# Kernel tuning notes

Measured on AMD Instinct MI355X. Metric: run time of the kernel, lower is better.

Reference implementation:

```python
import jax, jax.numpy as jnp
import numpy as np

EPS = 1e-5  # torch BatchNorm1d default eps


def _bn_train(h, gamma, beta):
    # BatchNorm1d in training mode over the edge (batch) axes: biased variance.
    m = jnp.mean(h, axis=(0, 1), keepdims=True)
    v = jnp.mean(jnp.square(h - m), axis=(0, 1), keepdims=True)
    return (h - m) * jax.lax.rsqrt(v + EPS) * gamma + beta


def setup_inputs() -> dict:
    key = jax.random.key(0)
    ks = jax.random.split(key, 12)
    N, F, H = 1024, 128, 128
    s1 = 1.0 / np.sqrt(2 * F)
    s2 = 1.0 / np.sqrt(H)
    return {
        "x": jax.random.normal(ks[0], (N, F), dtype=jnp.float32),
        "W1": jax.random.uniform(ks[1], (H, 2 * F), jnp.float32, -s1, s1),
        "b1": jax.random.uniform(ks[2], (H,), jnp.float32, -s1, s1),
        "W2": jax.random.uniform(ks[3], (H, H), jnp.float32, -s2, s2),
        "b2": jax.random.uniform(ks[4], (H,), jnp.float32, -s2, s2),
        "W3": jax.random.uniform(ks[5], (1, H), jnp.float32, -s2, s2),
        "b3": jax.random.uniform(ks[6], (1,), jnp.float32, -s2, s2),
        "g1": jnp.ones((H,), jnp.float32),
        "be1": jnp.zeros((H,), jnp.float32),
        "g2": jnp.ones((H,), jnp.float32),
        "be2": jnp.zeros((H,), jnp.float32),
    }


def reference(x, W1, b1, W2, b2, W3, b3, g1, be1, g2, be2):
    N, F = x.shape
    # Edge e = i*N + j pairs [x[j], x[i]] (row=j varies fast, col=i slow).
    # First Linear on the concat splits into two low-rank GEMMs + broadcast add,
    # avoiding the [N^2, 2F] materialization (same math as Linear(concat)).
    Wa, Wb = W1[:, :F], W1[:, F:]
    A = x @ Wa.T            # contribution of x[row] = x[j] -> varies over axis 1
    B = x @ Wb.T            # contribution of x[col] = x[i] -> varies over axis 0
    h = A[None, :, :] + B[:, None, :] + b1      # [N, N, H], h[i, j]
    h = jax.nn.relu(_bn_train(h, g1, be1))
    h = jnp.einsum('ijh,kh->ijk', h, W2) + b2   # [N, N, H]
    h = jax.nn.relu(_bn_train(h, g2, be2))
    logits = jnp.einsum('ijh,kh->ijk', h, W3)[..., 0] + b3[0]  # [N, N]
    adj = jax.nn.sigmoid((logits + logits.T) * 0.5)
    adj = adj - jnp.diag(jnp.diag(adj))
    return adj
```

## Files before the change

### kernel.cpp

```cpp
#include <hip/hip_runtime.h>
#include <hip/hip_bf16.h>

typedef __bf16 bf16x8 __attribute__((ext_vector_type(8)));
typedef float  f32x4  __attribute__((ext_vector_type(4)));
typedef float  f32x8  __attribute__((ext_vector_type(8)));

#define EPSV 1e-5f

__global__ __launch_bounds__(256) void k_ab(const float* __restrict__ x,
                                            const float* __restrict__ W1,
                                            const float* __restrict__ W2,
                                            float* __restrict__ A,
                                            float* __restrict__ Bm,
                                            float* __restrict__ gs,
                                            unsigned int* __restrict__ w2p) {
  __shared__ float xs[4 * 128];
  int t = threadIdx.x;
  if (blockIdx.x >= 256) {
    int c = (blockIdx.x - 256) * 256 + t;
    int pair = c & 3;
    int col  = (c >> 2) & 15;
    int quad = (c >> 6) & 3;
    int nt   = (c >> 8) & 7;
    int ks   = (c >> 11) & 3;
    int k = nt * 16 + col;
    int hch = ks * 32 + quad * 8 + pair * 2;
    __bf16 b0 = (__bf16)W2[k * 128 + hch];
    __bf16 b1 = (__bf16)W2[k * 128 + hch + 1];
    unsigned int u0 = *(unsigned short*)&b0, u1 = *(unsigned short*)&b1;
    w2p[c] = u0 | (u1 << 16);
    return;
  }
  int j0 = blockIdx.x * 4;
  for (int idx = t; idx < 512; idx += 256) xs[idx] = x[j0 * 128 + idx];
  __syncthreads();
  int h = t & 127, half = t >> 7;
  const float4* wrow = (const float4*)(W1 + h * 256 + half * 128);
  const float4* xs4 = (const float4*)xs;
  float a0 = 0.f, a1 = 0.f, a2 = 0.f, a3 = 0.f;
#pragma unroll 8
  for (int ch = 0; ch < 32; ++ch) {
    float4 wv = wrow[ch];
    float4 x0 = xs4[ch], x1 = xs4[32 + ch], x2 = xs4[64 + ch], x3 = xs4[96 + ch];
    a0 += wv.x * x0.x + wv.y * x0.y + wv.z * x0.z + wv.w * x0.w;
    a1 += wv.x * x1.x + wv.y * x1.y + wv.z * x1.z + wv.w * x1.w;
    a2 += wv.x * x2.x + wv.y * x2.y + wv.z * x2.z + wv.w * x2.w;
    a3 += wv.x * x3.x + wv.y * x3.y + wv.z * x3.z + wv.w * x3.w;
  }
  float* dst = half ? Bm : A;
  dst[(j0 + 0) * 128 + h] = a0;
  dst[(j0 + 1) * 128 + h] = a1;
  dst[(j0 + 2) * 128 + h] = a2;
  dst[(j0 + 3) * 128 + h] = a3;
  float s = a0 + a1 + a2 + a3;
  float q = a0 * a0 + a1 * a1 + a2 * a2 + a3 * a3;
  atomicAdd(&gs[half * 256 + h], s);
  atomicAdd(&gs[half * 256 + 128 + h], q);
}

__global__ __launch_bounds__(256) void k_fold_apply(const float* __restrict__ gs,
                                                    const float* __restrict__ g1,
                                                    const float* __restrict__ be1,
                                                    const float* __restrict__ A,
                                                    const float* __restrict__ Bm,
                                                    float* __restrict__ Ap,
                                                    float* __restrict__ Bt) {
  __shared__ float sc_s[128], ta_s[128], tb_s[128];
  int t = threadIdx.x;
  if (t < 128) {
    const float inv = 1.f / 1024.f;
    float mA = gs[t] * inv;
    float vA = gs[128 + t] * inv - mA * mA;
    float mB = gs[256 + t] * inv;
    float vB = gs[384 + t] * inv - mB * mB;
    float sc = g1[t] * rsqrtf(vA + vB + EPSV);
    sc_s[t] = sc;
    ta_s[t] = be1[t] - mA * sc;
    tb_s[t] = -mB * sc;
  }
  __syncthreads();
  int idx4 = blockIdx.x * 256 + t;
  int c4 = idx4 & 31;
  float4 sc = ((const float4*)sc_s)[c4];
  float4 ta = ((const float4*)ta_s)[c4];
  float4 tb = ((const float4*)tb_s)[c4];
  float4 a = ((const float4*)A)[idx4];
  float4 b = ((const float4*)Bm)[idx4];
  float4 oa, ob;
  oa.x = fmaf(a.x, sc.x, ta.x); oa.y = fmaf(a.y, sc.y, ta.y);
  oa.z = fmaf(a.z, sc.z, ta.z); oa.w = fmaf(a.w, sc.w, ta.w);
  ob.x = fmaf(b.x, sc.x, tb.x); ob.y = fmaf(b.y, sc.y, tb.y);
  ob.z = fmaf(b.z, sc.z, tb.z); ob.w = fmaf(b.w, sc.w, tb.w);
  int j = idx4 >> 5;
  int h4 = c4 << 2;
  int S = j >> 6, r = (j >> 4) & 3, col = j & 15;
  int ks = h4 >> 5, q = (h4 >> 3) & 3, eh = (h4 >> 2) & 1;
  int dst4 = S * 2048 + eh * 1024 + (r * 4 + ks) * 64 + q * 16 + col;
  ((float4*)Ap)[dst4] = oa;
  ((float4*)Bt)[idx4] = ob;
}

__device__ __forceinline__ bf16x8 build2(f32x4 alo, f32x4 ahi,
                                         const float* __restrict__ bp) {
  f32x4 b0 = *(const f32x4*)bp;
  f32x4 b1 = *(const f32x4*)(bp + 4);
  f32x4 z = {0.f, 0.f, 0.f, 0.f};
  f32x4 h0 = __builtin_elementwise_max(alo + b0, z);
  f32x4 h1 = __builtin_elementwise_max(ahi + b1, z);
  f32x8 h = __builtin_shufflevector(h0, h1, 0, 1, 2, 3, 4, 5, 6, 7);
  return __builtin_convertvector(h, bf16x8);
}

template <int PASS>
__global__ __launch_bounds__(256) void k_pass(
    const float* __restrict__ Ap, const float* __restrict__ Bt,
    const unsigned int* __restrict__ w2p, float* __restrict__ partials,
    const float* __restrict__ sum2, const float* __restrict__ g2,
    const float* __restrict__ be2, const float* __restrict__ W3v,
    const float* __restrict__ b3p, float* __restrict__ L) {
  __shared__ float lds[8192 + 1024];
  float* btl = lds + 8192;
  int t = threadIdx.x;
  int bid = blockIdx.x;
  int bj = bid & 15, bi = bid >> 4;
  int lane = t & 63, w = t >> 6;
  int col = lane & 15, quad = lane >> 4;

  const float* atsrc = Ap + bj * 8192;
#pragma unroll
  for (int it = 0; it < 8; ++it) {
    int g = w * 8 + it;
    __builtin_amdgcn_global_load_lds(
        (const __attribute__((address_space(1))) unsigned int*)(atsrc + g * 256 + lane * 4),
        (__attribute__((address_space(3))) unsigned int*)(lds + g * 256),
        16, 0, 0);
  }
  __builtin_amdgcn_global_load_lds(
      (const __attribute__((address_space(1))) unsigned int*)(Bt + (bi * 8 + w * 2) * 128 + lane * 4),
      (__attribute__((address_space(3))) unsigned int*)(btl + w * 256),
      16, 0, 0);

  bf16x8 bw[4][8];
#pragma unroll
  for (int ks = 0; ks < 4; ++ks)
#pragma unroll
    for (int nt = 0; nt < 8; ++nt)
      bw[ks][nt] = *(const bf16x8*)((const __bf16*)w2p + (((ks * 8 + nt) * 64) + lane) * 8);

  float s1[8], s2[8];
  float al[8], uu[8], w3l[8];
  float b3v = 0.f;
  if (PASS == 1) {
#pragma unroll
    for (int nt = 0; nt < 8; ++nt) { s1[nt] = 0.f; s2[nt] = 0.f; }
  } else {
    b3v = b3p[0];
    const float invM = 1.f / (1024.f * 1024.f);
#pragma unroll
    for (int nt = 0; nt < 8; ++nt) {
      int k = nt * 16 + col;
      float mdot = sum2[k] * invM;
      float var = sum2[128 + k] * invM - mdot * mdot;
      float alv = g2[k] * rsqrtf(var + EPSV);
      al[nt] = alv;
      uu[nt] = be2[k] - mdot * alv;
      w3l[nt] = W3v[k];
    }
  }
  __syncthreads();

  const float* bp0 = btl + w * 256;
  const float* bp1 = bp0 + 128;

  for (int s = 0; s < 4; ++s) {
    f32x4 acc[2][8];
#pragma unroll
    for (int mt = 0; mt < 2; ++mt)
#pragma unroll
      for (int nt = 0; nt < 8; ++nt) acc[mt][nt] = (f32x4){0.f, 0.f, 0.f, 0.f};

#pragma unroll
    for (int ks = 0; ks < 4; ++ks) {
      const float* ap = lds + ((s * 4 + ks) * 64 + lane) * 4;
      f32x4 alo = *(const f32x4*)ap;
      f32x4 ahi = *(const f32x4*)(ap + 4096);
      bf16x8 a0 = build2(alo, ahi, bp0 + ks * 32 + quad * 8);
      bf16x8 a1 = build2(alo, ahi, bp1 + ks * 32 + quad * 8);
#pragma unroll
      for (int nt = 0; nt < 8; ++nt) {
        acc[0][nt] = __builtin_amdgcn_mfma_f32_16x16x32_bf16(a0, bw[ks][nt], acc[0][nt], 0, 0, 0);
        acc[1][nt] = __builtin_amdgcn_mfma_f32_16x16x32_bf16(a1, bw[ks][nt], acc[1][nt], 0, 0, 0);
      }
    }

    if (PASS == 1) {
#pragma unroll
      for (int nt = 0; nt < 8; ++nt)
#pragma unroll
        for (int mt = 0; mt < 2; ++mt)
#pragma unroll
          for (int r = 0; r < 4; ++r) {
            float d = acc[mt][nt][r];
            s1[nt] += d;
            s2[nt] = fmaf(d, d, s2[nt]);
          }
    } else {
#pragma unroll
      for (int mt = 0; mt < 2; ++mt) {
        float rsum[4] = {0.f, 0.f, 0.f, 0.f};
#pragma unroll
        for (int nt = 0; nt < 8; ++nt)
#pragma unroll
          for (int r = 0; r < 4; ++r) {
            float h = fmaxf(fmaf(acc[mt][nt][r], al[nt], uu[nt]), 0.f);
            rsum[r] = fmaf(h, w3l[nt], rsum[r]);
          }
#pragma unroll
        for (int r = 0; r < 4; ++r) {
          rsum[r] += __shfl_xor(rsum[r], 1);
          rsum[r] += __shfl_xor(rsum[r], 2);
          rsum[r] += __shfl_xor(rsum[r], 4);
          rsum[r] += __shfl_xor(rsum[r], 8);
        }
        if (col == 0) {
          int i = bi * 8 + w * 2 + mt;
#pragma unroll
          for (int r = 0; r < 4; ++r)
            L[i * 1024 + bj * 64 + s * 16 + quad * 4 + r] = rsum[r] + b3v;
        }
      }
    }
  }

  if (PASS == 1) {
#pragma unroll
    for (int nt = 0; nt < 8; ++nt) {
      s1[nt] += __shfl_xor(s1[nt], 16);
      s1[nt] += __shfl_xor(s1[nt], 32);
      s2[nt] += __shfl_xor(s2[nt], 16);
      s2[nt] += __shfl_xor(s2[nt], 32);
    }
    __syncthreads();
    if (lane < 16) {
#pragma unroll
      for (int nt = 0; nt < 8; ++nt) {
        lds[w * 256 + nt * 16 + lane] = s1[nt];
        lds[w * 256 + 128 + nt * 16 + lane] = s2[nt];
      }
    }
    __syncthreads();
    float tot = lds[t] + lds[256 + t] + lds[512 + t] + lds[768 + t];
    partials[bid * 256 + t] = tot;
  }
}

__global__ __launch_bounds__(256) void k_red_partials(const float* __restrict__ partials,
                                                      float* __restrict__ sum2) {
  int t = threadIdx.x;
  float s = 0.f;
  int r0 = blockIdx.x * 16;
#pragma unroll
  for (int r = 0; r < 16; ++r) s += partials[(r0 + r) * 256 + t];
  atomicAdd(&sum2[t], s);
}

__global__ __launch_bounds__(256) void k_adj(const float* __restrict__ L,
                                             float* __restrict__ out) {
  int idx = blockIdx.x * 256 + threadIdx.x;
  int i = idx >> 10, j = idx & 1023;
  float a = L[i * 1024 + j];
  float b = L[j * 1024 + i];
  float s = 1.f / (1.f + __expf(-0.5f * (a + b)));
  out[idx] = (i == j) ? 0.f : s;
}

extern "C" void kernel_launch(void* const* d_in, const int* in_sizes, int n_in,
                              void* d_out, int out_size, void* d_ws, size_t ws_size,
                              hipStream_t stream) {
  const float* x   = (const float*)d_in[0];
  const float* W1  = (const float*)d_in[1];
  const float* W2  = (const float*)d_in[3];
  const float* W3  = (const float*)d_in[5];
  const float* b3  = (const float*)d_in[6];
  const float* g1  = (const float*)d_in[7];
  const float* be1 = (const float*)d_in[8];
  const float* g2  = (const float*)d_in[9];
  const float* be2 = (const float*)d_in[10];

  float* ws = (float*)d_ws;
  float* A        = ws;
  float* Bm       = ws + 131072;
  float* Ap       = ws + 262144;
  float* Bt       = ws + 393216;
  unsigned int* w2p = (unsigned int*)(ws + 524288);
  float* gs       = ws + 532480;
  float* sum2     = ws + 532992;
  float* partials = ws + 533248;
  float* L        = ws + 1057536;
  float* out      = (float*)d_out;

  hipMemsetAsync(gs, 0, 768 * sizeof(float), stream);

  k_ab<<<288, 256, 0, stream>>>(x, W1, W2, A, Bm, gs, w2p);
  k_fold_apply<<<128, 256, 0, stream>>>(gs, g1, be1, A, Bm, Ap, Bt);
  k_pass<1><<<2048, 256, 0, stream>>>(Ap, Bt, w2p, partials, nullptr, nullptr, nullptr, nullptr, nullptr, nullptr);
  k_red_partials<<<128, 256, 0, stream>>>(partials, sum2);
  k_pass<2><<<2048, 256, 0, stream>>>(Ap, Bt, w2p, nullptr, sum2, g2, be2, W3, b3, L);
  k_adj<<<4096, 256, 0, stream>>>(L, out);
}
```

Measured before the change: 225.3 us.

## Keep Bt rows in registers as packed bf16 and prefetch A fragments

Measured after the change: 229.8 us. No clear change (+2.0%).

```diff
diff --git a/kernel.cpp b/kernel.cpp
--- a/kernel.cpp
+++ b/kernel.cpp
@@ -100,13 +100,19 @@
   ((float4*)Bt)[idx4] = ob;
 }
 
-__device__ __forceinline__ bf16x8 build2(f32x4 alo, f32x4 ahi,
-                                         const float* __restrict__ bp) {
-  f32x4 b0 = *(const f32x4*)bp;
-  f32x4 b1 = *(const f32x4*)(bp + 4);
+__device__ __forceinline__ bf16x8 build_bt(f32x4 alo, f32x4 ahi, uint4 bt) {
+  f32x4 blo, bhi;
+  blo[0] = __uint_as_float(bt.x << 16);
+  blo[1] = __uint_as_float(bt.x & 0xffff0000u);
+  blo[2] = __uint_as_float(bt.y << 16);
+  blo[3] = __uint_as_float(bt.y & 0xffff0000u);
+  bhi[0] = __uint_as_float(bt.z << 16);
+  bhi[1] = __uint_as_float(bt.z & 0xffff0000u);
+  bhi[2] = __uint_as_float(bt.w << 16);
+  bhi[3] = __uint_as_float(bt.w & 0xffff0000u);
   f32x4 z = {0.f, 0.f, 0.f, 0.f};
-  f32x4 h0 = __builtin_elementwise_max(alo + b0, z);
-  f32x4 h1 = __builtin_elementwise_max(ahi + b1, z);
+  f32x4 h0 = __builtin_elementwise_max(alo + blo, z);
+  f32x4 h1 = __builtin_elementwise_max(ahi + bhi, z);
   f32x8 h = __builtin_shufflevector(h0, h1, 0, 1, 2, 3, 4, 5, 6, 7);
   return __builtin_convertvector(h, bf16x8);
 }
@@ -118,8 +124,7 @@
     const float* __restrict__ sum2, const float* __restrict__ g2,
     const float* __restrict__ be2, const float* __restrict__ W3v,
     const float* __restrict__ b3p, float* __restrict__ L) {
-  __shared__ float lds[8192 + 1024];
-  float* btl = lds + 8192;
+  __shared__ float lds[8192];
   int t = threadIdx.x;
   int bid = blockIdx.x;
   int bj = bid & 15, bi = bid >> 4;
@@ -135,10 +140,21 @@
         (__attribute__((address_space(3))) unsigned int*)(lds + g * 256),
         16, 0, 0);
   }
-  __builtin_amdgcn_global_load_lds(
-      (const __attribute__((address_space(1))) unsigned int*)(Bt + (bi * 8 + w * 2) * 128 + lane * 4),
-      (__attribute__((address_space(3))) unsigned int*)(btl + w * 256),
-      16, 0, 0);
+
+  uint4 btu[2][4];
+  {
+    const float* br = Bt + (bi * 8 + w * 2) * 128;
+#pragma unroll
+    for (int r = 0; r < 2; ++r)
+#pragma unroll
+      for (int ks = 0; ks < 4; ++ks) {
+        f32x4 lo = *(const f32x4*)(br + r * 128 + ks * 32 + quad * 8);
+        f32x4 hi = *(const f32x4*)(br + r * 128 + ks * 32 + quad * 8 + 4);
+        f32x8 v = __builtin_shufflevector(lo, hi, 0, 1, 2, 3, 4, 5, 6, 7);
+        bf16x8 b = __builtin_convertvector(v, bf16x8);
+        btu[r][ks] = *(uint4*)&b;
+      }
+  }
 
   bf16x8 bw[4][8];
 #pragma unroll
@@ -169,9 +185,6 @@
   }
   __syncthreads();
 
-  const float* bp0 = btl + w * 256;
-  const float* bp1 = bp0 + 128;
-
   for (int s = 0; s < 4; ++s) {
     f32x4 acc[2][8];
 #pragma unroll
@@ -179,18 +192,26 @@
 #pragma unroll
       for (int nt = 0; nt < 8; ++nt) acc[mt][nt] = (f32x4){0.f, 0.f, 0.f, 0.f};
 
+    const float* ap0 = lds + (s * 4 * 64 + lane) * 4;
+    f32x4 alo = *(const f32x4*)ap0;
+    f32x4 ahi = *(const f32x4*)(ap0 + 4096);
 #pragma unroll
     for (int ks = 0; ks < 4; ++ks) {
-      const float* ap = lds + ((s * 4 + ks) * 64 + lane) * 4;
-      f32x4 alo = *(const f32x4*)ap;
-      f32x4 ahi = *(const f32x4*)(ap + 4096);
-      bf16x8 a0 = build2(alo, ahi, bp0 + ks * 32 + quad * 8);
-      bf16x8 a1 = build2(alo, ahi, bp1 + ks * 32 + quad * 8);
+      f32x4 nlo, nhi;
+      if (ks < 3) {
+        const float* apn = lds + (((s * 4 + ks + 1) * 64) + lane) * 4;
+        nlo = *(const f32x4*)apn;
+        nhi = *(const f32x4*)(apn + 4096);
+      }
+      bf16x8 a0 = build_bt(alo, ahi, btu[0][ks]);
+      bf16x8 a1 = build_bt(alo, ahi, btu[1][ks]);
 #pragma unroll
       for (int nt = 0; nt < 8; ++nt) {
         acc[0][nt] = __builtin_amdgcn_mfma_f32_16x16x32_bf16(a0, bw[ks][nt], acc[0][nt], 0, 0, 0);
         acc[1][nt] = __builtin_amdgcn_mfma_f32_16x16x32_bf16(a1, bw[ks][nt], acc[1][nt], 0, 0, 0);
       }
+      alo = nlo;
+      ahi = nhi;
     }
 
     if (PASS == 1) {
```

## Fuse BN1 fold into pass kernels and replace partials reduction with atomics

Applied to the files above, without the earlier changes.

Result: slower. 246.4 us (+9.4%).

```diff
diff --git a/kernel.cpp b/kernel.cpp
--- a/kernel.cpp
+++ b/kernel.cpp
@@ -10,7 +10,7 @@
 __global__ __launch_bounds__(256) void k_ab(const float* __restrict__ x,
                                             const float* __restrict__ W1,
                                             const float* __restrict__ W2,
-                                            float* __restrict__ A,
+                                            float* __restrict__ Ap,
                                             float* __restrict__ Bm,
                                             float* __restrict__ gs,
                                             unsigned int* __restrict__ w2p) {
@@ -47,26 +47,71 @@
     a2 += wv.x * x2.x + wv.y * x2.y + wv.z * x2.z + wv.w * x2.w;
     a3 += wv.x * x3.x + wv.y * x3.y + wv.z * x3.z + wv.w * x3.w;
   }
-  float* dst = half ? Bm : A;
-  dst[(j0 + 0) * 128 + h] = a0;
-  dst[(j0 + 1) * 128 + h] = a1;
-  dst[(j0 + 2) * 128 + h] = a2;
-  dst[(j0 + 3) * 128 + h] = a3;
+  if (half == 0) {
+    int S = j0 >> 6, r16 = (j0 >> 4) & 3, colj = j0 & 15;
+    int ks = h >> 5, q = (h >> 3) & 3, eh = (h >> 2) & 1, pos = h & 3;
+    int base = S * 8192 + eh * 4096 + (r16 * 4 + ks) * 256 + q * 64 + colj * 4 + pos;
+    Ap[base] = a0;
+    Ap[base + 4] = a1;
+    Ap[base + 8] = a2;
+    Ap[base + 12] = a3;
+  } else {
+    Bm[(j0 + 0) * 128 + h] = a0;
+    Bm[(j0 + 1) * 128 + h] = a1;
+    Bm[(j0 + 2) * 128 + h] = a2;
+    Bm[(j0 + 3) * 128 + h] = a3;
+  }
   float s = a0 + a1 + a2 + a3;
-  float q = a0 * a0 + a1 * a1 + a2 * a2 + a3 * a3;
+  float q2 = a0 * a0 + a1 * a1 + a2 * a2 + a3 * a3;
   atomicAdd(&gs[half * 256 + h], s);
-  atomicAdd(&gs[half * 256 + 128 + h], q);
-}
-
-__global__ __launch_bounds__(256) void k_fold_apply(const float* __restrict__ gs,
-                                                    const float* __restrict__ g1,
-                                                    const float* __restrict__ be1,
-                                                    const float* __restrict__ A,
-                                                    const float* __restrict__ Bm,
-                                                    float* __restrict__ Ap,
-                                                    float* __restrict__ Bt) {
-  __shared__ float sc_s[128], ta_s[128], tb_s[128];
+  atomicAdd(&gs[half * 256 + 128 + h], q2);
+}
+
+__device__ __forceinline__ bf16x8 build_fold(f32x4 alo, f32x4 ahi,
+                                             const float* __restrict__ bp,
+                                             f32x4 sl, f32x4 sh,
+                                             f32x4 tl, f32x4 th) {
+  f32x4 b0 = *(const f32x4*)bp;
+  f32x4 b1 = *(const f32x4*)(bp + 4);
+  f32x4 z = {0.f, 0.f, 0.f, 0.f};
+  f32x4 h0 = __builtin_elementwise_max((alo + b0) * sl + tl, z);
+  f32x4 h1 = __builtin_elementwise_max((ahi + b1) * sh + th, z);
+  f32x8 h = __builtin_shufflevector(h0, h1, 0, 1, 2, 3, 4, 5, 6, 7);
+  return __builtin_convertvector(h, bf16x8);
+}
+
+template <int PASS>
+__global__ __launch_bounds__(256) void k_pass(
+    const float* __restrict__ Ap, const float* __restrict__ Bm,
+    const unsigned int* __restrict__ w2p,
+    const float* __restrict__ gs, const float* __restrict__ g1,
+    const float* __restrict__ be1,
+    float* __restrict__ sum2, const float* __restrict__ g2,
+    const float* __restrict__ be2, const float* __restrict__ W3v,
+    const float* __restrict__ b3p, float* __restrict__ L) {
+  __shared__ float lds[8192 + 1024 + 256];
+  float* btl = lds + 8192;
+  float* prm = lds + 9216;
   int t = threadIdx.x;
+  int bid = blockIdx.x;
+  int bj = bid & 15, bi = bid >> 4;
+  int lane = t & 63, w = t >> 6;
+  int col = lane & 15, quad = lane >> 4;
+
+  const float* atsrc = Ap + bj * 8192;
+#pragma unroll
+  for (int it = 0; it < 8; ++it) {
+    int g = w * 8 + it;
+    __builtin_amdgcn_global_load_lds(
+        (const __attribute__((address_space(1))) unsigned int*)(atsrc + g * 256 + lane * 4),
+        (__attribute__((address_space(3))) unsigned int*)(lds + g * 256),
+        16, 0, 0);
+  }
+  __builtin_amdgcn_global_load_lds(
+      (const __attribute__((address_space(1))) unsigned int*)(Bm + (bi * 8 + w * 2) * 128 + lane * 4),
+      (__attribute__((address_space(3))) unsigned int*)(btl + w * 256),
+      16, 0, 0);
+
   if (t < 128) {
     const float inv = 1.f / 1024.f;
     float mA = gs[t] * inv;
@@ -74,71 +119,9 @@
     float mB = gs[256 + t] * inv;
     float vB = gs[384 + t] * inv - mB * mB;
     float sc = g1[t] * rsqrtf(vA + vB + EPSV);
-    sc_s[t] = sc;
-    ta_s[t] = be1[t] - mA * sc;
-    tb_s[t] = -mB * sc;
-  }
-  __syncthreads();
-  int idx4 = blockIdx.x * 256 + t;
-  int c4 = idx4 & 31;
-  float4 sc = ((const float4*)sc_s)[c4];
-  float4 ta = ((const float4*)ta_s)[c4];
-  float4 tb = ((const float4*)tb_s)[c4];
-  float4 a = ((const float4*)A)[idx4];
-  float4 b = ((const float4*)Bm)[idx4];
-  float4 oa, ob;
-  oa.x = fmaf(a.x, sc.x, ta.x); oa.y = fmaf(a.y, sc.y, ta.y);
-  oa.z = fmaf(a.z, sc.z, ta.z); oa.w = fmaf(a.w, sc.w, ta.w);
-  ob.x = fmaf(b.x, sc.x, tb.x); ob.y = fmaf(b.y, sc.y, tb.y);
-  ob.z = fmaf(b.z, sc.z, tb.z); ob.w = fmaf(b.w, sc.w, tb.w);
-  int j = idx4 >> 5;
-  int h4 = c4 << 2;
-  int S = j >> 6, r = (j >> 4) & 3, col = j & 15;
-  int ks = h4 >> 5, q = (h4 >> 3) & 3, eh = (h4 >> 2) & 1;
-  int dst4 = S * 2048 + eh * 1024 + (r * 4 + ks) * 64 + q * 16 + col;
-  ((float4*)Ap)[dst4] = oa;
-  ((float4*)Bt)[idx4] = ob;
-}
-
-__device__ __forceinline__ bf16x8 build2(f32x4 alo, f32x4 ahi,
-                                         const float* __restrict__ bp) {
-  f32x4 b0 = *(const f32x4*)bp;
-  f32x4 b1 = *(const f32x4*)(bp + 4);
-  f32x4 z = {0.f, 0.f, 0.f, 0.f};
-  f32x4 h0 = __builtin_elementwise_max(alo + b0, z);
-  f32x4 h1 = __builtin_elementwise_max(ahi + b1, z);
-  f32x8 h = __builtin_shufflevector(h0, h1, 0, 1, 2, 3, 4, 5, 6, 7);
-  return __builtin_convertvector(h, bf16x8);
-}
-
-template <int PASS>
-__global__ __launch_bounds__(256) void k_pass(
-    const float* __restrict__ Ap, const float* __restrict__ Bt,
-    const unsigned int* __restrict__ w2p, float* __restrict__ partials,
-    const float* __restrict__ sum2, const float* __restrict__ g2,
-    const float* __restrict__ be2, const float* __restrict__ W3v,
-    const float* __restrict__ b3p, float* __restrict__ L) {
-  __shared__ float lds[8192 + 1024];
-  float* btl = lds + 8192;
-  int t = threadIdx.x;
-  int bid = blockIdx.x;
-  int bj = bid & 15, bi = bid >> 4;
-  int lane = t & 63, w = t >> 6;
-  int col = lane & 15, quad = lane >> 4;
-
-  const float* atsrc = Ap + bj * 8192;
-#pragma unroll
-  for (int it = 0; it < 8; ++it) {
-    int g = w * 8 + it;
-    __builtin_amdgcn_global_load_lds(
-        (const __attribute__((address_space(1))) unsigned int*)(atsrc + g * 256 + lane * 4),
-        (__attribute__((address_space(3))) unsigned int*)(lds + g * 256),
-        16, 0, 0);
-  }
-  __builtin_amdgcn_global_load_lds(
-      (const __attribute__((address_space(1))) unsigned int*)(Bt + (bi * 8 + w * 2) * 128 + lane * 4),
-      (__attribute__((address_space(3))) unsigned int*)(btl + w * 256),
-      16, 0, 0);
+    prm[t] = sc;
+    prm[128 + t] = be1[t] - (mA + mB) * sc;
+  }
 
   bf16x8 bw[4][8];
 #pragma unroll
@@ -184,8 +167,13 @@
       const float* ap = lds + ((s * 4 + ks) * 64 + lane) * 4;
       f32x4 alo = *(const f32x4*)ap;
       f32x4 ahi = *(const f32x4*)(ap + 4096);
-      bf16x8 a0 = build2(alo, ahi, bp0 + ks * 32 + quad * 8);
-      bf16x8 a1 = build2(alo, ahi, bp1 + ks * 32 + quad * 8);
+      int po = ks * 32 + quad * 8;
+      f32x4 sl = *(const f32x4*)(prm + po);
+      f32x4 sh = *(const f32x4*)(prm + po + 4);
+      f32x4 tl = *(const f32x4*)(prm + 128 + po);
+      f32x4 th = *(const f32x4*)(prm + 128 + po + 4);
+      bf16x8 a0 = build_fold(alo, ahi, bp0 + po, sl, sh, tl, th);
+      bf16x8 a1 = build_fold(alo, ahi, bp1 + po, sl, sh, tl, th);
 #pragma unroll
       for (int nt = 0; nt < 8; ++nt) {
         acc[0][nt] = __builtin_amdgcn_mfma_f32_16x16x32_bf16(a0, bw[ks][nt], acc[0][nt], 0, 0, 0);
@@ -224,9 +212,9 @@
         }
         if (col == 0) {
           int i = bi * 8 + w * 2 + mt;
-#pragma unroll
-          for (int r = 0; r < 4; ++r)
-            L[i * 1024 + bj * 64 + s * 16 + quad * 4 + r] = rsum[r] + b3v;
+          float4 v = make_float4(rsum[0] + b3v, rsum[1] + b3v,
+                                 rsum[2] + b3v, rsum[3] + b3v);
+          *(float4*)(&L[i * 1024 + bj * 64 + s * 16 + quad * 4]) = v;
         }
       }
     }
@@ -250,18 +238,8 @@
     }
     __syncthreads();
     float tot = lds[t] + lds[256 + t] + lds[512 + t] + lds[768 + t];
-    partials[bid * 256 + t] = tot;
-  }
-}
-
-__global__ __launch_bounds__(256) void k_red_partials(const float* __restrict__ partials,
-                                                      float* __restrict__ sum2) {
-  int t = threadIdx.x;
-  float s = 0.f;
-  int r0 = blockIdx.x * 16;
-#pragma unroll
-  for (int r = 0; r < 16; ++r) s += partials[(r0 + r) * 256 + t];
-  atomicAdd(&sum2[t], s);
+    atomicAdd(&sum2[t], tot);
+  }
 }
 
 __global__ __launch_bounds__(256) void k_adj(const float* __restrict__ L,
@@ -288,23 +266,20 @@
   const float* be2 = (const float*)d_in[10];
 
   float* ws = (float*)d_ws;
-  float* A        = ws;
+  float* Ap       = ws;
   float* Bm       = ws + 131072;
-  float* Ap       = ws + 262144;
-  float* Bt       = ws + 393216;
-  unsigned int* w2p = (unsigned int*)(ws + 524288);
-  float* gs       = ws + 532480;
-  float* sum2     = ws + 532992;
-  float* partials = ws + 533248;
-  float* L        = ws + 1057536;
+  unsigned int* w2p = (unsigned int*)(ws + 262144);
+  float* gs       = ws + 270336;
+  float* sum2     = ws + 270848;
+  float* L        = ws + 271104;
   float* out      = (float*)d_out;
 
   hipMemsetAsync(gs, 0, 768 * sizeof(float), stream);
 
-  k_ab<<<288, 256, 0, stream>>>(x, W1, W2, A, Bm, gs, w2p);
-  k_fold_apply<<<128, 256, 0, stream>>>(gs, g1, be1, A, Bm, Ap, Bt);
-  k_pass<1><<<2048, 256, 0, stream>>>(Ap, Bt, w2p, partials, nullptr, nullptr, nullptr, nullptr, nullptr, nullptr);
-  k_red_partials<<<128, 256, 0, stream>>>(partials, sum2);
-  k_pass<2><<<2048, 256, 0, stream>>>(Ap, Bt, w2p, nullptr, sum2, g2, be2, W3, b3, L);
+  k_ab<<<288, 256, 0, stream>>>(x, W1, W2, Ap, Bm, gs, w2p);
+  k_pass<1><<<2048, 256, 0, stream>>>(Ap, Bm, w2p, gs, g1, be1, sum2,
+                                      nullptr, nullptr, nullptr, nullptr, nullptr);
+  k_pass<2><<<2048, 256, 0, stream>>>(Ap, Bm, w2p, gs, g1, be1, sum2,
+                                      g2, be2, W3, b3, L);
   k_adj<<<4096, 256, 0, stream>>>(L, out);
 }
```
